# Performance work log

Measured on AMD Instinct MI355X. Metric: run time of the kernel, lower is better.

## Reference

```python
import jax, jax.numpy as jnp
import numpy as np

LOG2 = float(np.log(2.0))

def shifted_softplus(x):
    return jax.nn.softplus(x) - LOG2

def setup_inputs() -> dict:
    key = jax.random.key(0)
    ks = jax.random.split(key, 12)
    N, E = 100000, 1600000
    Cin, Cout, F_, G = 128, 128, 128, 50
    x = jax.random.normal(ks[0], (N, Cin), dtype=jnp.float32)
    edge_index = jax.random.randint(ks[1], (2, E), 0, N, dtype=jnp.int64)
    edge_attr = jax.random.uniform(ks[2], (E, G), dtype=jnp.float32)
    s = lambda fan_in: 1.0 / np.sqrt(fan_in)
    lin1_w = jax.random.uniform(ks[3], (F_, Cin), jnp.float32, -s(Cin), s(Cin))
    lin1_b = jax.random.uniform(ks[4], (F_,), jnp.float32, -s(Cin), s(Cin))
    lin2_w = jax.random.uniform(ks[5], (Cout, F_), jnp.float32, -s(F_), s(F_))
    lin2_b = jax.random.uniform(ks[6], (Cout,), jnp.float32, -s(F_), s(F_))
    fn1_w = jax.random.uniform(ks[7], (F_, G), jnp.float32, -s(G), s(G))
    fn1_b = jax.random.uniform(ks[8], (F_,), jnp.float32, -s(G), s(G))
    fn2_w = jax.random.uniform(ks[9], (F_, F_), jnp.float32, -s(F_), s(F_))
    fn2_b = jax.random.uniform(ks[10], (F_,), jnp.float32, -s(F_), s(F_))
    return {"x": x, "edge_index": edge_index, "edge_attr": edge_attr,
            "lin1_w": lin1_w, "lin1_b": lin1_b, "lin2_w": lin2_w, "lin2_b": lin2_b,
            "fn1_w": fn1_w, "fn1_b": fn1_b, "fn2_w": fn2_w, "fn2_b": fn2_b}

def reference(x, edge_index, edge_attr, lin1_w, lin1_b, lin2_w, lin2_b,
              fn1_w, fn1_b, fn2_w, fn2_b):
    row, col = edge_index[0], edge_index[1]
    # filter network: [E, G] -> [E, F]
    W = shifted_softplus(edge_attr @ fn1_w.T + fn1_b) @ fn2_w.T + fn2_b
    # transform nodes then gather source features: [E, F]
    x_j = (x @ lin1_w.T + lin1_b)[col]
    msg = x_j * W
    # scatter-add over destination nodes: [N, F]
    agg = jax.ops.segment_sum(msg, row, num_segments=x.shape[0])
    return agg @ lin2_w.T + lin2_b
```

## Files before the change

### kernel.cpp

```cpp
#include <hip/hip_runtime.h>

#define NN 100000
#define NE 1600000
#define CC 128
#define GG 50
#define EPB 128
#define NSCB 98

typedef _Float16 half8 __attribute__((ext_vector_type(8)));
typedef _Float16 half2v __attribute__((ext_vector_type(2)));
typedef float f32x4 __attribute__((ext_vector_type(4)));

static __device__ __forceinline__ f32x4 mfma16(half8 a, half8 b, f32x4 c) {
    return __builtin_amdgcn_mfma_f32_16x16x32_f16(a, b, c, 0, 0, 0);
}

__global__ __launch_bounds__(256) void pack_frags(const float* fn1_w, const float* fn2_w,
                                                  _Float16* ws_frag)
{
    int tid = threadIdx.x;
    for (int s = tid; s < 1024; s += 256) {
        int l = s & 63, ks = (s >> 6) & 1, nb = s >> 7;
        int f = nb * 16 + (l & 15);
        int k0 = ks * 32 + 8 * (l >> 4);
        half8 v;
        #pragma unroll
        for (int i = 0; i < 8; i++) {
            int g = k0 + i;
            v[i] = (g < GG) ? (_Float16)fn1_w[f * GG + g] : (_Float16)0.f;
        }
        *reinterpret_cast<half8*>(&ws_frag[s * 8]) = v;
    }
    for (int s = tid; s < 2048; s += 256) {
        int l = s & 63, ks = (s >> 6) & 3, nb = s >> 8;
        int f = (l & 15) * 8 + nb;
        int k0 = ks * 32 + 8 * (l >> 4);
        const float* wp = fn2_w + f * CC + k0;
        half8 v;
        #pragma unroll
        for (int i = 0; i < 8; i++) v[i] = (_Float16)wp[i];
        *reinterpret_cast<half8*>(&ws_frag[8192 + s * 8]) = v;
    }
}

template <typename InT, typename OutT, bool DOH>
__global__ __launch_bounds__(256) void lin_kernel(const InT* in, const float* w,
                                                  const float* bias, OutT* out, int nrows,
                                                  const int* hrow, int* hcnt)
{
    __shared__ __align__(16) _Float16 a_lds[64][136];
    __shared__ __align__(16) _Float16 bfrag[2048 * 8];

    int tid = threadIdx.x;
    int rowBase = blockIdx.x * 64;

    if constexpr (sizeof(InT) == 4) {
        for (int i = tid; i < 64 * 32; i += 256) {
            int r = i >> 5, c4 = i & 31;
            float4 v = {0.f, 0.f, 0.f, 0.f};
            if (rowBase + r < nrows)
                v = reinterpret_cast<const float4*>(in)[(size_t)(rowBase + r) * (CC / 4) + c4];
            a_lds[r][c4 * 4 + 0] = (_Float16)v.x;
            a_lds[r][c4 * 4 + 1] = (_Float16)v.y;
            a_lds[r][c4 * 4 + 2] = (_Float16)v.z;
            a_lds[r][c4 * 4 + 3] = (_Float16)v.w;
        }
    } else {
        for (int i = tid; i < 64 * 16; i += 256) {
            int r = i >> 4, c8 = i & 15;
            half8 v;
            #pragma unroll
            for (int k = 0; k < 8; k++) v[k] = (_Float16)0.f;
            if (rowBase + r < nrows)
                v = reinterpret_cast<const half8*>(in)[(size_t)(rowBase + r) * (CC / 8) + c8];
            *reinterpret_cast<half8*>(&a_lds[r][c8 * 8]) = v;
        }
    }
    for (int s = tid; s < 2048; s += 256) {
        int l = s & 63, ks = (s >> 6) & 3, nb = s >> 8;
        int f = nb * 16 + (l & 15);
        int k0 = ks * 32 + 8 * (l >> 4);
        const float* wp = w + f * CC + k0;
        half8 v;
        #pragma unroll
        for (int i = 0; i < 8; i++) v[i] = (_Float16)wp[i];
        *reinterpret_cast<half8*>(&bfrag[s * 8]) = v;
    }

    if constexpr (DOH) {
        int idx4 = blockIdx.x * 256 + tid;
        if (idx4 < NE / 4) {
            int4 e4 = reinterpret_cast<const int4*>(hrow)[idx4];
            atomicAdd(&hcnt[e4.x], 1);
            atomicAdd(&hcnt[e4.y], 1);
            atomicAdd(&hcnt[e4.z], 1);
            atomicAdd(&hcnt[e4.w], 1);
        }
    }
    __syncthreads();

    int wid = tid >> 6, l = tid & 63;
    int lr = l & 15, lg = l >> 4;
    int wrow = wid * 16;

    half8 afr[4];
    #pragma unroll
    for (int ks = 0; ks < 4; ks++)
        afr[ks] = *reinterpret_cast<const half8*>(&a_lds[wrow + lr][ks * 32 + 8 * lg]);

    #pragma unroll
    for (int nb = 0; nb < 8; nb++) {
        f32x4 acc = {0.f, 0.f, 0.f, 0.f};
        #pragma unroll
        for (int ks = 0; ks < 4; ks++) {
            half8 bf = *reinterpret_cast<const half8*>(&bfrag[((nb * 4 + ks) * 64 + l) * 8]);
            acc = mfma16(afr[ks], bf, acc);
        }
        float bv = bias[nb * 16 + lr];
        #pragma unroll
        for (int j = 0; j < 4; j++) {
            int r = rowBase + wrow + lg * 4 + j;
            if (r < nrows) out[(size_t)r * CC + nb * 16 + lr] = (OutT)(acc[j] + bv);
        }
    }
}

__global__ __launch_bounds__(256) void scanA(const int* cnt, int* excl, int* bsum, int n) {
    __shared__ int lds[256];
    int b = blockIdx.x, t = threadIdx.x;
    int base = b * 1024 + t * 4;
    int v[4];
    #pragma unroll
    for (int i = 0; i < 4; i++) v[i] = (base + i < n) ? cnt[base + i] : 0;
    int s = v[0] + v[1] + v[2] + v[3];
    lds[t] = s;
    __syncthreads();
    for (int off = 1; off < 256; off <<= 1) {
        int x = (t >= off) ? lds[t - off] : 0;
        __syncthreads();
        lds[t] += x;
        __syncthreads();
    }
    int incl = lds[t];
    int run = incl - s;
    #pragma unroll
    for (int i = 0; i < 4; i++) {
        if (base + i < n) excl[base + i] = run;
        run += v[i];
    }
    if (t == 255) bsum[b] = incl;
}

__global__ __launch_bounds__(128) void scanB(int* bsum, int n) {
    __shared__ int lds[128];
    int t = threadIdx.x;
    int v = (t < n) ? bsum[t] : 0;
    lds[t] = v;
    __syncthreads();
    for (int off = 1; off < 128; off <<= 1) {
        int x = (t >= off) ? lds[t - off] : 0;
        __syncthreads();
        lds[t] += x;
        __syncthreads();
    }
    if (t < n) bsum[t] = lds[t] - v;
}

__global__ __launch_bounds__(256) void scanC(int* excl, const int* bsum, int* cursor, int n) {
    int b = blockIdx.x, t = threadIdx.x;
    int off = bsum[b];
    int base = b * 1024 + t * 4;
    #pragma unroll
    for (int i = 0; i < 4; i++) {
        int idx = base + i;
        if (idx < n) {
            int val = excl[idx] + off;
            excl[idx] = val;
            cursor[idx] = val;
        }
    }
}

__global__ __launch_bounds__(512, 8) void msg_scatter_kernel(
    const _Float16* __restrict__ x1, const int* __restrict__ eidx,
    const float* __restrict__ ea, const _Float16* __restrict__ frag_ws,
    const float* __restrict__ fn1_b, const float* __restrict__ fn2_b,
    int* __restrict__ cursor, _Float16* __restrict__ msg)
{
    __shared__ __align__(16) unsigned char u_lds[EPB * CC * 2];
    __shared__ int cols_l[EPB];
    __shared__ int p_l[EPB];

    int tid = threadIdx.x;
    size_t eBase = (size_t)blockIdx.x * EPB;

    if (tid < EPB) {
        int r = eidx[eBase + tid];
        cols_l[tid] = eidx[(size_t)NE + eBase + tid];
        p_l[tid] = atomicAdd(&cursor[r], 1);
    }
    {
        const float2* eap = reinterpret_cast<const float2*>(ea + eBase * GG);
        for (int i = tid; i < EPB * 25; i += 512) {
            int e = i / 25, g2 = i - e * 25;
            float2 v = eap[i];
            int byte = e * 128 + ((g2 * 4) ^ ((e & 7) << 4));
            _Float16* p = reinterpret_cast<_Float16*>(u_lds + byte);
            p[0] = (_Float16)v.x;
            p[1] = (_Float16)v.y;
        }
        for (int i = tid; i < EPB * 14; i += 512) {
            int e = i / 14, g = (i - e * 14) + 50;
            int byte = e * 128 + ((g * 2) ^ ((e & 7) << 4));
            *reinterpret_cast<_Float16*>(u_lds + byte) = (_Float16)0.f;
        }
    }
    __syncthreads();

    int wv = tid >> 6, l = tid & 63;
    int lr = l & 15, lg = l >> 4;
    int erow = wv * 16;

    half8 a1[2];
    #pragma unroll
    for (int ks = 0; ks < 2; ks++) {
        int e = erow + lr;
        int byte = e * 128 + ((ks * 64 + lg * 16) ^ ((e & 7) << 4));
        a1[ks] = *reinterpret_cast<const half8*>(u_lds + byte);
    }
    __syncthreads();

    #pragma unroll
    for (int nb = 0; nb < 8; nb++) {
        half8 b10 = *reinterpret_cast<const half8*>(&frag_ws[((nb * 2 + 0) * 64 + l) * 8]);
        half8 b11 = *reinterpret_cast<const half8*>(&frag_ws[((nb * 2 + 1) * 64 + l) * 8]);
        f32x4 acc = {0.f, 0.f, 0.f, 0.f};
        acc = mfma16(a1[0], b10, acc);
        acc = mfma16(a1[1], b11, acc);
        float bv = fn1_b[nb * 16 + lr];
        int f = nb * 16 + lr;
        #pragma unroll
        for (int j = 0; j < 4; j++) {
            float z = acc[j] + bv;
            float t = __expf(-fabsf(z));
            float hz = fmaxf(z, 0.f) + __logf(1.f + t) - 0.69314718055994531f;
            int e = erow + lg * 4 + j;
            int byte = e * 256 + ((f * 2) ^ ((e & 7) << 4));
            *reinterpret_cast<_Float16*>(u_lds + byte) = (_Float16)hz;
        }
    }
    __syncthreads();

    half8 a2[4];
    #pragma unroll
    for (int ks = 0; ks < 4; ks++) {
        int e = erow + lr;
        int byte = e * 256 + ((ks * 64 + lg * 16) ^ ((e & 7) << 4));
        a2[ks] = *reinterpret_cast<const half8*>(u_lds + byte);
    }
    int pp[4], cc4[4];
    #pragma unroll
    for (int j = 0; j < 4; j++) {
        int e = erow + lg * 4 + j;
        pp[j] = p_l[e];
        cc4[j] = cols_l[e];
    }

    const half8* b2g = reinterpret_cast<const half8*>(frag_ws + 8192);
    #pragma unroll
    for (int hf = 0; hf < 2; hf++) {
        f32x4 acc[4];
        #pragma unroll
        for (int q = 0; q < 4; q++) {
            int nb = hf * 4 + q;
            f32x4 a = {0.f, 0.f, 0.f, 0.f};
            #pragma unroll
            for (int ks = 0; ks < 4; ks++)
                a = mfma16(a2[ks], b2g[(nb * 4 + ks) * 64 + l], a);
            acc[q] = a;
        }
        int ch0 = lr * 8 + hf * 4;
        float4 bv = *reinterpret_cast<const float4*>(&fn2_b[ch0]);

        #pragma unroll
        for (int j = 0; j < 4; j++) {
            uint2 xp = *reinterpret_cast<const uint2*>(&x1[(size_t)cc4[j] * CC + ch0]);
            half2v x01 = __builtin_bit_cast(half2v, xp.x);
            half2v x23 = __builtin_bit_cast(half2v, xp.y);
            half2v p0, p1;
            p0[0] = (_Float16)((float)x01[0] * (acc[0][j] + bv.x));
            p0[1] = (_Float16)((float)x01[1] * (acc[1][j] + bv.y));
            p1[0] = (_Float16)((float)x23[0] * (acc[2][j] + bv.z));
            p1[1] = (_Float16)((float)x23[1] * (acc[3][j] + bv.w));
            uint2 st;
            st.x = __builtin_bit_cast(unsigned, p0);
            st.y = __builtin_bit_cast(unsigned, p1);
            *reinterpret_cast<uint2*>(&msg[(size_t)pp[j] * CC + ch0]) = st;
        }
    }
}

__global__ __launch_bounds__(512, 8) void gather_reduce_kernel(
    const _Float16* __restrict__ msg, const int* __restrict__ rowptr,
    _Float16* __restrict__ aggH)
{
    int tid = threadIdx.x;
    int r = blockIdx.x * 8 + (tid >> 6);
    int l = tid & 63;
    int e0 = rowptr[r];
    int e1 = (r == NN - 1) ? NE : rowptr[r + 1];

    const unsigned* base = reinterpret_cast<const unsigned*>(msg) + l;
    float a0 = 0.f, a1 = 0.f;
    int i = e0;
    for (; i + 1 < e1; i += 2) {
        unsigned v0 = base[(size_t)i * 64];
        unsigned v1 = base[(size_t)(i + 1) * 64];
        half2v h0 = __builtin_bit_cast(half2v, v0);
        half2v h1 = __builtin_bit_cast(half2v, v1);
        a0 += (float)h0[0] + (float)h1[0];
        a1 += (float)h0[1] + (float)h1[1];
    }
    if (i < e1) {
        half2v h = __builtin_bit_cast(half2v, base[(size_t)i * 64]);
        a0 += (float)h[0];
        a1 += (float)h[1];
    }
    half2v o;
    o[0] = (_Float16)a0;
    o[1] = (_Float16)a1;
    reinterpret_cast<unsigned*>(aggH)[(size_t)r * 64 + l] = __builtin_bit_cast(unsigned, o);
}

__global__ __launch_bounds__(512, 8) void edge_kernel_atomic(
    const _Float16* __restrict__ x1, const int* __restrict__ eidx,
    const float* __restrict__ ea, const _Float16* __restrict__ frag_ws,
    const float* __restrict__ fn1_b, const float* __restrict__ fn2_b,
    float* __restrict__ agg)
{
    __shared__ __align__(16) unsigned char u_lds[EPB * CC * 2];
    __shared__ int rows_l[EPB];
    __shared__ int cols_l[EPB];

    int tid = threadIdx.x;
    size_t eBase = (size_t)blockIdx.x * EPB;

    if (tid < EPB) {
        rows_l[tid] = eidx[eBase + tid];
        cols_l[tid] = eidx[(size_t)NE + eBase + tid];
    }
    {
        const float2* eap = reinterpret_cast<const float2*>(ea + eBase * GG);
        for (int i = tid; i < EPB * 25; i += 512) {
            int e = i / 25, g2 = i - e * 25;
            float2 v = eap[i];
            int byte = e * 128 + ((g2 * 4) ^ ((e & 7) << 4));
            _Float16* p = reinterpret_cast<_Float16*>(u_lds + byte);
            p[0] = (_Float16)v.x;
            p[1] = (_Float16)v.y;
        }
        for (int i = tid; i < EPB * 14; i += 512) {
            int e = i / 14, g = (i - e * 14) + 50;
            int byte = e * 128 + ((g * 2) ^ ((e & 7) << 4));
            *reinterpret_cast<_Float16*>(u_lds + byte) = (_Float16)0.f;
        }
    }
    __syncthreads();

    int wv = tid >> 6, l = tid & 63;
    int lr = l & 15, lg = l >> 4;
    int erow = wv * 16;

    half8 a1[2];
    #pragma unroll
    for (int ks = 0; ks < 2; ks++) {
        int e = erow + lr;
        int byte = e * 128 + ((ks * 64 + lg * 16) ^ ((e & 7) << 4));
        a1[ks] = *reinterpret_cast<const half8*>(u_lds + byte);
    }
    __syncthreads();

    #pragma unroll
    for (int nb = 0; nb < 8; nb++) {
        half8 b10 = *reinterpret_cast<const half8*>(&frag_ws[((nb * 2 + 0) * 64 + l) * 8]);
        half8 b11 = *reinterpret_cast<const half8*>(&frag_ws[((nb * 2 + 1) * 64 + l) * 8]);
        f32x4 acc = {0.f, 0.f, 0.f, 0.f};
        acc = mfma16(a1[0], b10, acc);
        acc = mfma16(a1[1], b11, acc);
        float bv = fn1_b[nb * 16 + lr];
        int f = nb * 16 + lr;
        #pragma unroll
        for (int j = 0; j < 4; j++) {
            float z = acc[j] + bv;
            float t = __expf(-fabsf(z));
            float hz = fmaxf(z, 0.f) + __logf(1.f + t) - 0.69314718055994531f;
            int e = erow + lg * 4 + j;
            int byte = e * 256 + ((f * 2) ^ ((e & 7) << 4));
            *reinterpret_cast<_Float16*>(u_lds + byte) = (_Float16)hz;
        }
    }
    __syncthreads();

    half8 a2[4];
    #pragma unroll
    for (int ks = 0; ks < 4; ks++) {
        int e = erow + lr;
        int byte = e * 256 + ((ks * 64 + lg * 16) ^ ((e & 7) << 4));
        a2[ks] = *reinterpret_cast<const half8*>(u_lds + byte);
    }
    int rr[4], cc4[4];
    #pragma unroll
    for (int j = 0; j < 4; j++) {
        int e = erow + lg * 4 + j;
        rr[j] = rows_l[e];
        cc4[j] = cols_l[e];
    }
    const half8* b2g = reinterpret_cast<const half8*>(frag_ws + 8192);
    #pragma unroll
    for (int hf = 0; hf < 2; hf++) {
        f32x4 acc[4];
        #pragma unroll
        for (int q = 0; q < 4; q++) {
            int nb = hf * 4 + q;
            f32x4 a = {0.f, 0.f, 0.f, 0.f};
            #pragma unroll
            for (int ks = 0; ks < 4; ks++)
                a = mfma16(a2[ks], b2g[(nb * 4 + ks) * 64 + l], a);
            acc[q] = a;
        }
        int ch0 = lr * 8 + hf * 4;
        float4 bv = *reinterpret_cast<const float4*>(&fn2_b[ch0]);
        #pragma unroll
        for (int j = 0; j < 4; j++) {
            uint2 xp = *reinterpret_cast<const uint2*>(&x1[(size_t)cc4[j] * CC + ch0]);
            half2v x01 = __builtin_bit_cast(half2v, xp.x);
            half2v x23 = __builtin_bit_cast(half2v, xp.y);
            float* dst = &agg[(size_t)rr[j] * CC + ch0];
            atomicAdd(dst + 0, (float)x01[0] * (acc[0][j] + bv.x));
            atomicAdd(dst + 1, (float)x01[1] * (acc[1][j] + bv.y));
            atomicAdd(dst + 2, (float)x23[0] * (acc[2][j] + bv.z));
            atomicAdd(dst + 3, (float)x23[1] * (acc[3][j] + bv.w));
        }
    }
}

extern "C" void kernel_launch(void* const* d_in, const int* in_sizes, int n_in,
                              void* d_out, int out_size, void* d_ws, size_t ws_size,
                              hipStream_t stream) {
    const float* x      = (const float*)d_in[0];
    const int*   eidx   = (const int*)d_in[1];
    const float* ea     = (const float*)d_in[2];
    const float* lin1_w = (const float*)d_in[3];
    const float* lin1_b = (const float*)d_in[4];
    const float* lin2_w = (const float*)d_in[5];
    const float* lin2_b = (const float*)d_in[6];
    const float* fn1_w  = (const float*)d_in[7];
    const float* fn1_b  = (const float*)d_in[8];
    const float* fn2_w  = (const float*)d_in[9];
    const float* fn2_b  = (const float*)d_in[10];

    float* out = (float*)d_out;

    const size_t o_frag = 0;
    const size_t o_x1h  = 65536;
    const size_t o_msg  = o_x1h + (size_t)NN * CC * 2;
    const size_t o_aggH = o_msg + (size_t)NE * CC * 2;
    const size_t o_cnt  = o_aggH + (size_t)NN * CC * 2;
    const size_t o_rp   = o_cnt + (size_t)NN * 4;
    const size_t o_cur  = o_rp + (size_t)NN * 4;
    const size_t o_bsum = o_cur + (size_t)NN * 4;
    const size_t req    = o_bsum + 512;

    _Float16* frag_ws = (_Float16*)((char*)d_ws + o_frag);
    _Float16* x1h     = (_Float16*)((char*)d_ws + o_x1h);

    pack_frags<<<1, 256, 0, stream>>>(fn1_w, fn2_w, frag_ws);

    if (ws_size >= req) {
        _Float16* msg  = (_Float16*)((char*)d_ws + o_msg);
        _Float16* aggH = (_Float16*)((char*)d_ws + o_aggH);
        int* cnt    = (int*)((char*)d_ws + o_cnt);
        int* rowptr = (int*)((char*)d_ws + o_rp);
        int* cursor = (int*)((char*)d_ws + o_cur);
        int* bsum   = (int*)((char*)d_ws + o_bsum);

        hipMemsetAsync(cnt, 0, (size_t)NN * 4, stream);
        lin_kernel<float, _Float16, true><<<(NN + 63) / 64, 256, 0, stream>>>(
            x, lin1_w, lin1_b, x1h, NN, eidx, cnt);
        scanA<<<NSCB, 256, 0, stream>>>(cnt, rowptr, bsum, NN);
        scanB<<<1, 128, 0, stream>>>(bsum, NSCB);
        scanC<<<NSCB, 256, 0, stream>>>(rowptr, bsum, cursor, NN);

        msg_scatter_kernel<<<NE / EPB, 512, 0, stream>>>(x1h, eidx, ea, frag_ws,
                                                         fn1_b, fn2_b, cursor, msg);
        gather_reduce_kernel<<<NN / 8, 512, 0, stream>>>(msg, rowptr, aggH);
        lin_kernel<_Float16, float, false><<<(NN + 63) / 64, 256, 0, stream>>>(
            aggH, lin2_w, lin2_b, out, NN, nullptr, nullptr);
    } else {
        lin_kernel<float, _Float16, false><<<(NN + 63) / 64, 256, 0, stream>>>(
            x, lin1_w, lin1_b, x1h, NN, nullptr, nullptr);
        hipMemsetAsync(out, 0, (size_t)NN * CC * sizeof(float), stream);
        edge_kernel_atomic<<<NE / EPB, 512, 0, stream>>>(x1h, eidx, ea, frag_ws,
                                                         fn1_b, fn2_b, out);
        lin_kernel<float, float, false><<<(NN + 63) / 64, 256, 0, stream>>>(
            out, lin2_w, lin2_b, out, NN, nullptr, nullptr);
    }
}
```

Measured before the change: 708.8 us.

## Fuse segment reduction with lin2 matmul into one kernel

Merges the per-row gather-reduce kernel and the final lin2 linear kernel into one kernel. Each block reduces 64 destination rows into LDS as fp16, packs the lin2 weights into MFMA fragments in LDS, and computes the output tile with MFMA. This removes the aggH round trip through global memory and one launch. In exchange every block re-packs the full weight matrix from fp32, LDS use per block rises, and occupancy drops to 4 blocks.

```diff
diff --git a/kernel.cpp b/kernel.cpp
--- a/kernel.cpp
+++ b/kernel.cpp
@@ -300,36 +300,83 @@
     }
 }
 
-__global__ __launch_bounds__(512, 8) void gather_reduce_kernel(
+__global__ __launch_bounds__(512, 4) void reduce_lin2_kernel(
     const _Float16* __restrict__ msg, const int* __restrict__ rowptr,
-    _Float16* __restrict__ aggH)
+    const float* __restrict__ w, const float* __restrict__ bias,
+    float* __restrict__ out)
 {
+    __shared__ __align__(16) _Float16 a_lds[64][136];
+    __shared__ __align__(16) _Float16 bfrag[2048 * 8];
+
     int tid = threadIdx.x;
-    int r = blockIdx.x * 8 + (tid >> 6);
-    int l = tid & 63;
-    int e0 = rowptr[r];
-    int e1 = (r == NN - 1) ? NE : rowptr[r + 1];
-
-    const unsigned* base = reinterpret_cast<const unsigned*>(msg) + l;
-    float a0 = 0.f, a1 = 0.f;
-    int i = e0;
-    for (; i + 1 < e1; i += 2) {
-        unsigned v0 = base[(size_t)i * 64];
-        unsigned v1 = base[(size_t)(i + 1) * 64];
-        half2v h0 = __builtin_bit_cast(half2v, v0);
-        half2v h1 = __builtin_bit_cast(half2v, v1);
-        a0 += (float)h0[0] + (float)h1[0];
-        a1 += (float)h0[1] + (float)h1[1];
-    }
-    if (i < e1) {
-        half2v h = __builtin_bit_cast(half2v, base[(size_t)i * 64]);
-        a0 += (float)h[0];
-        a1 += (float)h[1];
-    }
-    half2v o;
-    o[0] = (_Float16)a0;
-    o[1] = (_Float16)a1;
-    reinterpret_cast<unsigned*>(aggH)[(size_t)r * 64 + l] = __builtin_bit_cast(unsigned, o);
+    int rowBase = blockIdx.x * 64;
+    int wv = tid >> 6, l = tid & 63;
+
+    for (int s = tid; s < 2048; s += 512) {
+        int ll = s & 63, ks = (s >> 6) & 3, nb = s >> 8;
+        int f = nb * 16 + (ll & 15);
+        int k0 = ks * 32 + 8 * (ll >> 4);
+        const float* wp = w + f * CC + k0;
+        half8 v;
+        #pragma unroll
+        for (int i = 0; i < 8; i++) v[i] = (_Float16)wp[i];
+        *reinterpret_cast<half8*>(&bfrag[s * 8]) = v;
+    }
+
+    for (int k = 0; k < 8; k++) {
+        int r = rowBase + wv * 8 + k;
+        float a0 = 0.f, a1 = 0.f;
+        if (r < NN) {
+            int e0 = rowptr[r];
+            int e1 = (r == NN - 1) ? NE : rowptr[r + 1];
+            const unsigned* base = reinterpret_cast<const unsigned*>(msg) + l;
+            int i = e0;
+            for (; i + 1 < e1; i += 2) {
+                unsigned v0 = base[(size_t)i * 64];
+                unsigned v1 = base[(size_t)(i + 1) * 64];
+                half2v h0 = __builtin_bit_cast(half2v, v0);
+                half2v h1 = __builtin_bit_cast(half2v, v1);
+                a0 += (float)h0[0] + (float)h1[0];
+                a1 += (float)h0[1] + (float)h1[1];
+            }
+            if (i < e1) {
+                half2v h = __builtin_bit_cast(half2v, base[(size_t)i * 64]);
+                a0 += (float)h[0];
+                a1 += (float)h[1];
+            }
+        }
+        half2v o;
+        o[0] = (_Float16)a0;
+        o[1] = (_Float16)a1;
+        *reinterpret_cast<half2v*>(&a_lds[wv * 8 + k][l * 2]) = o;
+    }
+    __syncthreads();
+
+    int wid2 = wv & 3, hf = wv >> 2;
+    int lr = l & 15, lg = l >> 4;
+    int wrow = wid2 * 16;
+
+    half8 afr[4];
+    #pragma unroll
+    for (int ks = 0; ks < 4; ks++)
+        afr[ks] = *reinterpret_cast<const half8*>(&a_lds[wrow + lr][ks * 32 + 8 * lg]);
+
+    #pragma unroll
+    for (int q = 0; q < 4; q++) {
+        int nb = hf * 4 + q;
+        f32x4 acc = {0.f, 0.f, 0.f, 0.f};
+        #pragma unroll
+        for (int ks = 0; ks < 4; ks++) {
+            half8 bf = *reinterpret_cast<const half8*>(&bfrag[((nb * 4 + ks) * 64 + l) * 8]);
+            acc = mfma16(afr[ks], bf, acc);
+        }
+        float bv = bias[nb * 16 + lr];
+        #pragma unroll
+        for (int j = 0; j < 4; j++) {
+            int r = rowBase + wrow + lg * 4 + j;
+            if (r < NN) out[(size_t)r * CC + nb * 16 + lr] = acc[j] + bv;
+        }
+    }
 }
 
 __global__ __launch_bounds__(512, 8) void edge_kernel_atomic(
@@ -464,8 +511,7 @@
     const size_t o_frag = 0;
     const size_t o_x1h  = 65536;
     const size_t o_msg  = o_x1h + (size_t)NN * CC * 2;
-    const size_t o_aggH = o_msg + (size_t)NE * CC * 2;
-    const size_t o_cnt  = o_aggH + (size_t)NN * CC * 2;
+    const size_t o_cnt  = o_msg + (size_t)NE * CC * 2;
     const size_t o_rp   = o_cnt + (size_t)NN * 4;
     const size_t o_cur  = o_rp + (size_t)NN * 4;
     const size_t o_bsum = o_cur + (size_t)NN * 4;
@@ -478,7 +524,6 @@
 
     if (ws_size >= req) {
         _Float16* msg  = (_Float16*)((char*)d_ws + o_msg);
-        _Float16* aggH = (_Float16*)((char*)d_ws + o_aggH);
         int* cnt    = (int*)((char*)d_ws + o_cnt);
         int* rowptr = (int*)((char*)d_ws + o_rp);
         int* cursor = (int*)((char*)d_ws + o_cur);
@@ -493,9 +538,8 @@
 
         msg_scatter_kernel<<<NE / EPB, 512, 0, stream>>>(x1h, eidx, ea, frag_ws,
                                                          fn1_b, fn2_b, cursor, msg);
-        gather_reduce_kernel<<<NN / 8, 512, 0, stream>>>(msg, rowptr, aggH);
-        lin_kernel<_Float16, float, false><<<(NN + 63) / 64, 256, 0, stream>>>(
-            aggH, lin2_w, lin2_b, out, NN, nullptr, nullptr);
+        reduce_lin2_kernel<<<(NN + 63) / 64, 512, 0, stream>>>(msg, rowptr,
+                                                               lin2_w, lin2_b, out);
     } else {
         lin_kernel<float, _Float16, false><<<(NN + 63) / 64, 256, 0, stream>>>(
             x, lin1_w, lin1_b, x1h, NN, nullptr, nullptr);
```

Result: slower. 740.3 us (+4.5%).
